# Optimization experiments

Hardware: AMD Instinct MI355X
Metric: run time of the kernel (lower is better)

## Reference

```python
import jax, jax.numpy as jnp
import numpy as np

CUTOFF = 4.0
RBF_N = 32          # distance_embedding_size == D_rbf
F_DIM = 128         # hidden_size
N_ATOMS = 20000
N_PROBES = 100000
N_EDGES = 262144
LN_EPS = 1e-5


def setup_inputs() -> dict:
    key = jax.random.key(0)
    ks = jax.random.split(key, 20)
    s = 0.02
    inp = {
        "diff_pi": jax.random.normal(ks[0], (N_EDGES, 3), jnp.float32),
        "S_JK": jax.random.normal(ks[1], (N_ATOMS, F_DIM), jnp.float32),
        "V_JK": jax.random.normal(ks[2], (N_ATOMS, 3, F_DIM), jnp.float32),
        "atom_idx": jax.random.randint(ks[3], (N_EDGES,), 0, N_ATOMS),
        "probe_idx": jax.random.randint(ks[4], (N_EDGES,), 0, N_PROBES),
        "num_probes": N_PROBES,
        # state branch params
        "w_s1": jax.random.normal(ks[5], (3 * F_DIM, F_DIM), jnp.float32) * s,
        "b_s1": jnp.zeros((F_DIM,), jnp.float32),
        "g_ln": jnp.ones((F_DIM,), jnp.float32),
        "b_ln": jnp.zeros((F_DIM,), jnp.float32),
        "w_s2": jax.random.normal(ks[6], (F_DIM, F_DIM), jnp.float32) * s,
        "b_s2": jnp.zeros((F_DIM,), jnp.float32),
        # filter branch params
        "w_f1": jax.random.normal(ks[7], (RBF_N, F_DIM), jnp.float32) * s,
        "b_f1": jnp.zeros((F_DIM,), jnp.float32),
        "w_f2": jax.random.normal(ks[8], (F_DIM, F_DIM), jnp.float32) * s,
        "b_f2": jnp.zeros((F_DIM,), jnp.float32),
        # output head params
        "w_o1": jax.random.normal(ks[9], (F_DIM, F_DIM // 2), jnp.float32) * s,
        "b_o1": jnp.zeros((F_DIM // 2,), jnp.float32),
        "w_o2": jax.random.normal(ks[10], (F_DIM // 2, 1), jnp.float32) * s,
        "b_o2": jnp.zeros((1,), jnp.float32),
        "final_bias": jnp.array([-6.1], jnp.float32),
    }
    return inp


def reference(diff_pi, S_JK, V_JK, atom_idx, probe_idx, num_probes,
              w_s1, b_s1, g_ln, b_ln, w_s2, b_s2,
              w_f1, b_f1, w_f2, b_f2,
              w_o1, b_o1, w_o2, b_o2, final_bias):
    silu = jax.nn.silu
    # edge distances
    sq = (diff_pi ** 2).sum(-1)                       # [E]
    dist = jnp.sqrt(sq)                               # [E] exact distance
    dist_safe = jnp.sqrt(sq + 1e-8)[:, None]          # [E,1]
    r_hat = diff_pi / dist_safe                       # [E,3]

    # sinc RBF expansion: sin(n*pi*d/cutoff)/d, n=1..RBF_N
    n = jnp.arange(1, RBF_N + 1, dtype=diff_pi.dtype) # [D]
    e_pi = jnp.sin(dist[:, None] * n * (jnp.pi / CUTOFF)) / dist[:, None]  # [E,D]

    # gather atom features to edges
    n_i = jnp.sqrt((V_JK ** 2).sum(1) + 1e-8)         # [N,F]
    n_e = n_i[atom_idx]                               # [E,F]
    V_e = V_JK[atom_idx]                              # [E,3,F]
    q_pi = (V_e * r_hat[:, :, None]).sum(1)           # [E,F]
    S_e = S_JK[atom_idx]                              # [E,F]

    # state branch: Linear -> LayerNorm -> SiLU -> Linear
    h = jnp.concatenate([S_e, n_e, q_pi], axis=-1)    # [E,3F]
    u = h @ w_s1 + b_s1                               # [E,F]
    mu = u.mean(-1, keepdims=True)
    var = ((u - mu) ** 2).mean(-1, keepdims=True)
    u_norm = (u - mu) / jnp.sqrt(var + LN_EPS) * g_ln + b_ln
    state = silu(u_norm) @ w_s2 + b_s2                # [E,F]

    # filter branch (no normalization -> absolute distance scale)
    W = silu(e_pi @ w_f1 + b_f1) @ w_f2 + b_f2        # [E,F]

    # fuse + output head
    m = (silu((W * state) @ w_o1 + b_o1) @ w_o2 + b_o2)[:, 0]  # [E]

    x = dist / CUTOFF
    env = 1.0 - 21.0 * x ** 5 + 35.0 * x ** 6 - 15.0 * x ** 7
    env = jnp.where(dist < CUTOFF, env, jnp.zeros_like(env))
    m_w = m * env

    # scatter-add to probes
    rho = jax.ops.segment_sum(m_w, probe_idx, num_segments=num_probes)
    return rho + final_bias[0]
```

## Files before the change

kernel.cpp:

```cpp
#include <hip/hip_runtime.h>

#define EPB     64
#define E_TOTAL 262144
#define NPROBE  100000
#define N_ATOMS 20000
#define NTAB    4096

#define ASTR   136
#define A2_O   0
#define S_O    8704
#define MPT_O  17408
#define LDS_SH 17920

#define WS1_O  0
#define WS2_O  49152
#define WO1_O  65536
#define WT_TOT 73728
#define PQ_O   73728
#define PQ_SH  (N_ATOMS * 512)
#define WTAB_OFF_B ((PQ_O + PQ_SH) * 2)

typedef __attribute__((ext_vector_type(8))) short          short8;
typedef __attribute__((ext_vector_type(8))) unsigned short ushort8;
typedef __attribute__((ext_vector_type(4))) float          floatx4;

#define MFMA16(a, b, c) __builtin_amdgcn_mfma_f32_16x16x32_bf16((a), (b), (c), 0, 0, 0)

__device__ __forceinline__ short f2bf(float x) {
    unsigned u = __builtin_bit_cast(unsigned, x);
    u = (u + 0x7FFFu + ((u >> 16) & 1u)) >> 16;
    return (short)(unsigned short)u;
}
__device__ __forceinline__ unsigned pk2(float lo, float hi) {
    return __builtin_amdgcn_perm(__builtin_bit_cast(unsigned, hi),
                                 __builtin_bit_cast(unsigned, lo), 0x07060302u);
}
__device__ __forceinline__ float bf2f(unsigned short u) {
    return __builtin_bit_cast(float, ((unsigned)u) << 16);
}
__device__ __forceinline__ float silu_f(float x) { return x / (1.0f + __expf(-x)); }

struct F8 { float v[8]; };
__device__ __forceinline__ F8 ld8(const float* __restrict__ p) {
    F8 r;
    const float4 a = *(const float4*)p;
    const float4 b = *(const float4*)(p + 4);
    r.v[0] = a.x; r.v[1] = a.y; r.v[2] = a.z; r.v[3] = a.w;
    r.v[4] = b.x; r.v[5] = b.y; r.v[6] = b.z; r.v[7] = b.w;
    return r;
}

__global__ void cfr_prep_w(const float* __restrict__ w_s1, const float* __restrict__ w_s2,
                           const float* __restrict__ w_o1,
                           const float* __restrict__ fb, float* __restrict__ out,
                           unsigned short* __restrict__ wt) {
    int i = blockIdx.x * 256 + threadIdx.x;
    if (i < NPROBE) out[i] = fb[0];
    if (i < WT_TOT) {
        float v;
        if (i < WS2_O)      { int n = i / 384, k = i - n * 384;          v = w_s1[k * 128 + n]; }
        else if (i < WO1_O) { int j = i - WS2_O, n = j >> 7, k = j & 127; v = w_s2[k * 128 + n]; }
        else                { int j = i - WO1_O, n = j >> 7, k = j & 127; v = w_o1[k * 64 + n]; }
        wt[i] = (unsigned short)f2bf(v);
    }
}

__global__ __launch_bounds__(128) void cfr_prep_wtab(
    const float* __restrict__ w_f1, const float* __restrict__ b_f1,
    const float* __restrict__ w_f2, const float* __restrict__ b_f2,
    float* __restrict__ wtab)
{
    __shared__ float ep[32];
    __shared__ float f1s[128];
    const int t = threadIdx.x, row = blockIdx.x;
    float d = fmaxf(row * (4.0f / NTAB), 1e-4f);
    if (t < 32) ep[t] = sinf(d * (t + 1) * 0.7853981633974483f) / d;
    __syncthreads();
    float f1 = b_f1[t];
#pragma unroll
    for (int k = 0; k < 32; ++k) f1 = fmaf(ep[k], w_f1[k * 128 + t], f1);
    f1s[t] = silu_f(f1);
    __syncthreads();
    float w = b_f2[t];
    for (int k = 0; k < 128; ++k) w = fmaf(f1s[k], w_f2[k * 128 + t], w);
    wtab[row * 128 + t] = w;
}

__global__ __launch_bounds__(256, 3) void cfr_prep_pq(
    const float* __restrict__ S, const float* __restrict__ V,
    const float* __restrict__ b_s1,
    const unsigned short* __restrict__ wt, unsigned short* __restrict__ pq)
{
    __shared__ __align__(16) unsigned short bufH[32 * 264];
    __shared__ __align__(16) unsigned short bufV[96 * 136];

    const int t    = threadIdx.x;
    const int a0   = blockIdx.x * 32;
    const int wave = t >> 6;
    const int lane = t & 63;
    const int q    = lane >> 4;
    const int c16  = lane & 15;

#pragma unroll
    for (int it = 0; it < 2; ++it) {
        int idx = it * 256 + t;
        int al = idx >> 4, f8 = (idx & 15) * 8;
        int a = a0 + al;
        ushort8 sS, sN, s0, s1, s2;
        if (a < N_ATOMS) {
            F8 s  = ld8(S + a * 128 + f8);
            F8 v0 = ld8(V + a * 384 + f8);
            F8 v1 = ld8(V + a * 384 + 128 + f8);
            F8 v2 = ld8(V + a * 384 + 256 + f8);
#pragma unroll
            for (int j = 0; j < 8; ++j) {
                sS[j] = (unsigned short)f2bf(s.v[j]);
                sN[j] = (unsigned short)f2bf(sqrtf(v0.v[j]*v0.v[j] + v1.v[j]*v1.v[j] + v2.v[j]*v2.v[j] + 1e-8f));
                s0[j] = (unsigned short)f2bf(v0.v[j]);
                s1[j] = (unsigned short)f2bf(v1.v[j]);
                s2[j] = (unsigned short)f2bf(v2.v[j]);
            }
        } else {
#pragma unroll
            for (int j = 0; j < 8; ++j) { sS[j]=0; sN[j]=0; s0[j]=0; s1[j]=0; s2[j]=0; }
        }
        *(ushort8*)&bufH[al * 264 + f8]        = sS;
        *(ushort8*)&bufH[al * 264 + 128 + f8]  = sN;
        *(ushort8*)&bufV[al * 136 + f8]        = s0;
        *(ushort8*)&bufV[(32 + al) * 136 + f8] = s1;
        *(ushort8*)&bufV[(64 + al) * 136 + f8] = s2;
    }
    __syncthreads();

    const floatx4 zero4 = {0.f, 0.f, 0.f, 0.f};
    float bs1c[2];
#pragma unroll
    for (int ni = 0; ni < 2; ++ni) bs1c[ni] = b_s1[wave * 32 + ni * 16 + c16];

    {
        floatx4 pacc[2][2];
#pragma unroll
        for (int mi = 0; mi < 2; ++mi) { pacc[mi][0] = zero4; pacc[mi][1] = zero4; }
#pragma unroll
        for (int kk = 0; kk < 8; ++kk) {
            short8 bfr[2], af[2];
#pragma unroll
            for (int ni = 0; ni < 2; ++ni) {
                int n = wave * 32 + ni * 16 + c16;
                bfr[ni] = *(const short8*)&wt[WS1_O + n * 384 + kk * 32 + q * 8];
            }
#pragma unroll
            for (int mi = 0; mi < 2; ++mi)
                af[mi] = *(const short8*)&bufH[(mi * 16 + c16) * 264 + kk * 32 + q * 8];
#pragma unroll
            for (int mi = 0; mi < 2; ++mi)
#pragma unroll
                for (int ni = 0; ni < 2; ++ni)
                    pacc[mi][ni] = MFMA16(af[mi], bfr[ni], pacc[mi][ni]);
        }
#pragma unroll
        for (int mi = 0; mi < 2; ++mi)
#pragma unroll
            for (int r = 0; r < 4; ++r) {
                int a = a0 + mi * 16 + q * 4 + r;
                if (a < N_ATOMS)
#pragma unroll
                    for (int ni = 0; ni < 2; ++ni) {
                        int col = wave * 32 + ni * 16 + c16;
                        pq[a * 512 + col] = (unsigned short)f2bf(pacc[mi][ni][r] + bs1c[ni]);
                    }
            }
    }

    short8 bq[4][2];
#pragma unroll
    for (int kk = 0; kk < 4; ++kk)
#pragma unroll
        for (int ni = 0; ni < 2; ++ni) {
            int n = wave * 32 + ni * 16 + c16;
            bq[kk][ni] = *(const short8*)&wt[WS1_O + n * 384 + 256 + kk * 32 + q * 8];
        }
#pragma unroll
    for (int d = 0; d < 3; ++d) {
        floatx4 qacc[2][2];
#pragma unroll
        for (int mi = 0; mi < 2; ++mi) { qacc[mi][0] = zero4; qacc[mi][1] = zero4; }
#pragma unroll
        for (int kk = 0; kk < 4; ++kk) {
            short8 af[2];
#pragma unroll
            for (int mi = 0; mi < 2; ++mi)
                af[mi] = *(const short8*)&bufV[(d * 32 + mi * 16 + c16) * 136 + kk * 32 + q * 8];
#pragma unroll
            for (int mi = 0; mi < 2; ++mi)
#pragma unroll
                for (int ni = 0; ni < 2; ++ni)
                    qacc[mi][ni] = MFMA16(af[mi], bq[kk][ni], qacc[mi][ni]);
        }
#pragma unroll
        for (int mi = 0; mi < 2; ++mi)
#pragma unroll
            for (int r = 0; r < 4; ++r) {
                int a = a0 + mi * 16 + q * 4 + r;
                if (a < N_ATOMS)
#pragma unroll
                    for (int ni = 0; ni < 2; ++ni) {
                        int col = wave * 32 + ni * 16 + c16;
                        pq[a * 512 + (1 + d) * 128 + col] = (unsigned short)f2bf(qacc[mi][ni][r]);
                    }
            }
    }
}

__global__ __launch_bounds__(256, 4) void cfr_main(
    const float* __restrict__ diff,
    const int* __restrict__ atom_idx, const int* __restrict__ probe_idx,
    const unsigned short* __restrict__ wt, const unsigned short* __restrict__ pq,
    const float* __restrict__ wtab,
    const float* __restrict__ g_ln, const float* __restrict__ b_ln,
    const float* __restrict__ b_s2, const float* __restrict__ b_o1,
    const float* __restrict__ w_o2, const float* __restrict__ b_o2,
    float* __restrict__ out)
{
    __shared__ __align__(16) unsigned short LDSu[LDS_SH];
    float* mpart = (float*)&LDSu[MPT_O];

    const int t    = threadIdx.x;
    const int e0   = blockIdx.x * EPB;
    const int wave = t >> 6;
    const int lane = t & 63;
    const int q    = lane >> 4;
    const int c16  = lane & 15;
    const floatx4 zero4 = {0.f, 0.f, 0.f, 0.f};

    const int el = t >> 2;
    const int c0 = (t & 3) * 32;
    float dist;

    {
        const int eg = e0 + el;
        const int a  = atom_idx[eg];
        float dx = diff[eg * 3 + 0], dy = diff[eg * 3 + 1], dz = diff[eg * 3 + 2];
        float sq = dx * dx + dy * dy + dz * dz;
        dist = sqrtf(sq);
        float rinv = rsqrtf(sq + 1e-8f);
        float rx = dx * rinv, ry = dy * rinv, rz = dz * rinv;

        const ushort8* pqr = (const ushort8*)(pq + a * 512 + c0);
        float u[32];
#pragma unroll
        for (int g = 0; g < 4; ++g) {
            ushort8 v = pqr[g];
#pragma unroll
            for (int j = 0; j < 8; ++j) u[g * 8 + j] = bf2f(v[j]);
        }
#pragma unroll
        for (int g = 0; g < 4; ++g) {
            ushort8 v = pqr[16 + g];
#pragma unroll
            for (int j = 0; j < 8; ++j) u[g * 8 + j] = fmaf(bf2f(v[j]), rx, u[g * 8 + j]);
        }
#pragma unroll
        for (int g = 0; g < 4; ++g) {
            ushort8 v = pqr[32 + g];
#pragma unroll
            for (int j = 0; j < 8; ++j) u[g * 8 + j] = fmaf(bf2f(v[j]), ry, u[g * 8 + j]);
        }
#pragma unroll
        for (int g = 0; g < 4; ++g) {
            ushort8 v = pqr[48 + g];
#pragma unroll
            for (int j = 0; j < 8; ++j) u[g * 8 + j] = fmaf(bf2f(v[j]), rz, u[g * 8 + j]);
        }
        float s = 0.f, s2 = 0.f;
#pragma unroll
        for (int j = 0; j < 32; ++j) { s += u[j]; s2 = fmaf(u[j], u[j], s2); }
        s  += __shfl_xor(s, 1);  s  += __shfl_xor(s, 2);
        s2 += __shfl_xor(s2, 1); s2 += __shfl_xor(s2, 2);
        float mu = s * (1.f / 128.f);
        float rstd = rsqrtf(s2 * (1.f / 128.f) - mu * mu + 1e-5f);
        const float4* gp = (const float4*)(g_ln + c0);
        const float4* bp = (const float4*)(b_ln + c0);
        unsigned pko[16];
#pragma unroll
        for (int g4 = 0; g4 < 8; ++g4) {
            float4 gg = gp[g4], bb = bp[g4];
            float y0 = silu_f((u[g4 * 4 + 0] - mu) * rstd * gg.x + bb.x);
            float y1 = silu_f((u[g4 * 4 + 1] - mu) * rstd * gg.y + bb.y);
            float y2 = silu_f((u[g4 * 4 + 2] - mu) * rstd * gg.z + bb.z);
            float y3 = silu_f((u[g4 * 4 + 3] - mu) * rstd * gg.w + bb.w);
            pko[g4 * 2 + 0] = pk2(y0, y1);
            pko[g4 * 2 + 1] = pk2(y2, y3);
        }
        uint4* dst = (uint4*)&LDSu[A2_O + el * ASTR + c0];
        dst[0] = make_uint4(pko[0], pko[1], pko[2], pko[3]);
        dst[1] = make_uint4(pko[4], pko[5], pko[6], pko[7]);
        dst[2] = make_uint4(pko[8], pko[9], pko[10], pko[11]);
        dst[3] = make_uint4(pko[12], pko[13], pko[14], pko[15]);
    }
    __syncthreads();

    {
        floatx4 sacc[4][2];
#pragma unroll
        for (int mi = 0; mi < 4; ++mi) { sacc[mi][0] = zero4; sacc[mi][1] = zero4; }
#pragma unroll
        for (int kk = 0; kk < 4; ++kk) {
            short8 a2f[4], b2[2];
#pragma unroll
            for (int ni = 0; ni < 2; ++ni) {
                int n = wave * 32 + ni * 16 + c16;
                b2[ni] = *(const short8*)&wt[WS2_O + n * 128 + kk * 32 + q * 8];
            }
#pragma unroll
            for (int mi = 0; mi < 4; ++mi)
                a2f[mi] = *(const short8*)&LDSu[A2_O + (mi * 16 + c16) * ASTR + kk * 32 + q * 8];
#pragma unroll
            for (int mi = 0; mi < 4; ++mi)
#pragma unroll
                for (int ni = 0; ni < 2; ++ni)
                    sacc[mi][ni] = MFMA16(a2f[mi], b2[ni], sacc[mi][ni]);
        }
        float bs2c[2];
#pragma unroll
        for (int ni = 0; ni < 2; ++ni) bs2c[ni] = b_s2[wave * 32 + ni * 16 + c16];
#pragma unroll
        for (int mi = 0; mi < 4; ++mi)
#pragma unroll
            for (int r = 0; r < 4; ++r) {
                int row = mi * 16 + q * 4 + r;
#pragma unroll
                for (int ni = 0; ni < 2; ++ni) {
                    float v = sacc[mi][ni][r] + bs2c[ni];
                    LDSu[S_O + row * ASTR + (wave * 32 + ni * 16 + c16)] =
                        (unsigned short)(__builtin_bit_cast(unsigned, v) >> 16);
                }
            }
    }
    __syncthreads();

    {
        float f  = fminf(dist * (NTAB / 4.0f), (float)(NTAB - 1));
        float fi = floorf(f);
        int   i0 = (int)fi;
        float fr = f - fi;
        const float* r0 = wtab + i0 * 128 + c0;
        const float* r1 = r0 + 128;
        float w0[32], w1[32];
#pragma unroll
        for (int g4 = 0; g4 < 8; ++g4) {
            *(float4*)&w0[g4 * 4] = *(const float4*)(r0 + g4 * 4);
            *(float4*)&w1[g4 * 4] = *(const float4*)(r1 + g4 * 4);
        }
        ushort8 sv[4];
#pragma unroll
        for (int g = 0; g < 4; ++g)
            sv[g] = *(const ushort8*)&LDSu[S_O + el * ASTR + c0 + g * 8];
        unsigned pko[16];
#pragma unroll
        for (int p = 0; p < 16; ++p) {
            int j0 = p * 2, j1 = p * 2 + 1;
            float wa = fmaf(fr, w1[j0] - w0[j0], w0[j0]);
            float wb = fmaf(fr, w1[j1] - w0[j1], w0[j1]);
            float ga = bf2f(sv[j0 >> 3][j0 & 7]) * wa;
            float gb = bf2f(sv[j1 >> 3][j1 & 7]) * wb;
            pko[p] = pk2(ga, gb);
        }
        uint4* dst = (uint4*)&LDSu[A2_O + el * ASTR + c0];
        dst[0] = make_uint4(pko[0], pko[1], pko[2], pko[3]);
        dst[1] = make_uint4(pko[4], pko[5], pko[6], pko[7]);
        dst[2] = make_uint4(pko[8], pko[9], pko[10], pko[11]);
        dst[3] = make_uint4(pko[12], pko[13], pko[14], pko[15]);
    }
    __syncthreads();

    {
        const int n2 = wave * 16 + c16;
        floatx4 oacc[4];
#pragma unroll
        for (int mi = 0; mi < 4; ++mi) oacc[mi] = zero4;
#pragma unroll
        for (int kk = 0; kk < 4; ++kk) {
            short8 bfr = *(const short8*)&wt[WO1_O + n2 * 128 + kk * 32 + q * 8];
#pragma unroll
            for (int mi = 0; mi < 4; ++mi) {
                short8 af = *(const short8*)&LDSu[A2_O + (mi * 16 + c16) * ASTR + kk * 32 + q * 8];
                oacc[mi] = MFMA16(af, bfr, oacc[mi]);
            }
        }
        float bo1c = b_o1[n2], wo2c = w_o2[n2];
#pragma unroll
        for (int mi = 0; mi < 4; ++mi)
#pragma unroll
            for (int r = 0; r < 4; ++r) {
                float s = silu_f(oacc[mi][r] + bo1c) * wo2c;
#pragma unroll
                for (int d = 1; d < 16; d <<= 1) s += __shfl_xor(s, d, 64);
                if (c16 == 0) mpart[(mi * 16 + q * 4 + r) * 4 + wave] = s;
            }
    }
    __syncthreads();

    if (t < EPB) {
        int eg = e0 + t;
        float m = mpart[t * 4 + 0] + mpart[t * 4 + 1] + mpart[t * 4 + 2] + mpart[t * 4 + 3] + b_o2[0];
        float dx = diff[eg * 3 + 0], dy = diff[eg * 3 + 1], dz = diff[eg * 3 + 2];
        float dd = sqrtf(dx * dx + dy * dy + dz * dz);
        float x  = dd * 0.25f;
        float x2 = x * x, x4 = x2 * x2;
        float x5 = x4 * x, x6 = x5 * x, x7 = x6 * x;
        float env = 1.0f - 21.0f * x5 + 35.0f * x6 - 15.0f * x7;
        env = (dd < 4.0f) ? env : 0.0f;
        float mw = m * env;
        if (mw != 0.f) unsafeAtomicAdd(&out[probe_idx[eg]], mw);
    }
}

extern "C" void kernel_launch(void* const* d_in, const int* in_sizes, int n_in,
                              void* d_out, int out_size, void* d_ws, size_t ws_size,
                              hipStream_t stream) {
    const float* diff    = (const float*)d_in[0];
    const float* S_JK    = (const float*)d_in[1];
    const float* V_JK    = (const float*)d_in[2];
    const int*   atom_i  = (const int*)d_in[3];
    const int*   probe_i = (const int*)d_in[4];
    const float* w_s1 = (const float*)d_in[6];
    const float* b_s1 = (const float*)d_in[7];
    const float* g_ln = (const float*)d_in[8];
    const float* b_ln = (const float*)d_in[9];
    const float* w_s2 = (const float*)d_in[10];
    const float* b_s2 = (const float*)d_in[11];
    const float* w_f1 = (const float*)d_in[12];
    const float* b_f1 = (const float*)d_in[13];
    const float* w_f2 = (const float*)d_in[14];
    const float* b_f2 = (const float*)d_in[15];
    const float* w_o1 = (const float*)d_in[16];
    const float* b_o1 = (const float*)d_in[17];
    const float* w_o2 = (const float*)d_in[18];
    const float* b_o2 = (const float*)d_in[19];
    const float* fbias = (const float*)d_in[20];
    float* out = (float*)d_out;

    unsigned short* wt  = (unsigned short*)d_ws;
    unsigned short* pqp = wt + PQ_O;
    float* wtab = (float*)((char*)d_ws + WTAB_OFF_B);

    cfr_prep_w<<<(NPROBE + 255) / 256, 256, 0, stream>>>(w_s1, w_s2, w_o1, fbias, out, wt);
    cfr_prep_wtab<<<NTAB + 1, 128, 0, stream>>>(w_f1, b_f1, w_f2, b_f2, wtab);
    cfr_prep_pq<<<(N_ATOMS + 31) / 32, 256, 0, stream>>>(S_JK, V_JK, b_s1, wt, pqp);
    cfr_main<<<E_TOTAL / EPB, 256, 0, stream>>>(diff, atom_i, probe_i, wt, pqp, wtab,
        g_ln, b_ln, b_s2, b_o1, w_o2, b_o2, out);
}
```

Baseline: 249.8 us.

## Sort edges by atom, pack bf16 filter table pairs, fuse filter into epilogue

Adds a counting sort of the edges by atom index (histogram, scan, scatter) so the per-edge gathers of the precomputed atom projections are grouped in memory. Diff and probe index are packed together into a float4 per sorted edge. The filter table is halved in size and stored as packed bf16 pairs of adjacent rows. The filter interpolation and multiply now happen directly in the state GEMM epilogue, which removes an LDS staging buffer and allows higher occupancy. The cost is four extra small kernels, extra workspace, lower table precision and a less spread-out pattern of atomics.

```diff
diff --git a/kernel.cpp b/kernel.cpp
--- a/kernel.cpp
+++ b/kernel.cpp
@@ -4,21 +4,23 @@
 #define E_TOTAL 262144
 #define NPROBE  100000
 #define N_ATOMS 20000
-#define NTAB    4096
+#define NTAB    2048
 
 #define ASTR   136
 #define A2_O   0
-#define S_O    8704
-#define MPT_O  17408
-#define LDS_SH 17920
+#define LDS_SH 8704
 
 #define WS1_O  0
 #define WS2_O  49152
 #define WO1_O  65536
 #define WT_TOT 73728
-#define PQ_O   73728
-#define PQ_SH  (N_ATOMS * 512)
-#define WTAB_OFF_B ((PQ_O + PQ_SH) * 2)
+#define PQ_B   147456
+#define WTI_B  20627456
+#define WTF_B  21676032
+#define CNT_B  22725120
+#define CUR_B  22805120
+#define SA_B   22885120
+#define ED_B   23933696
 
 typedef __attribute__((ext_vector_type(8))) short          short8;
 typedef __attribute__((ext_vector_type(8))) unsigned short ushort8;
@@ -26,10 +28,10 @@
 
 #define MFMA16(a, b, c) __builtin_amdgcn_mfma_f32_16x16x32_bf16((a), (b), (c), 0, 0, 0)
 
-__device__ __forceinline__ short f2bf(float x) {
+__device__ __forceinline__ unsigned short f2bfu(float x) {
     unsigned u = __builtin_bit_cast(unsigned, x);
     u = (u + 0x7FFFu + ((u >> 16) & 1u)) >> 16;
-    return (short)(unsigned short)u;
+    return (unsigned short)u;
 }
 __device__ __forceinline__ unsigned pk2(float lo, float hi) {
     return __builtin_amdgcn_perm(__builtin_bit_cast(unsigned, hi),
@@ -53,22 +55,67 @@
 __global__ void cfr_prep_w(const float* __restrict__ w_s1, const float* __restrict__ w_s2,
                            const float* __restrict__ w_o1,
                            const float* __restrict__ fb, float* __restrict__ out,
-                           unsigned short* __restrict__ wt) {
+                           unsigned short* __restrict__ wt, int* __restrict__ cnt) {
     int i = blockIdx.x * 256 + threadIdx.x;
     if (i < NPROBE) out[i] = fb[0];
+    if (i < N_ATOMS) cnt[i] = 0;
     if (i < WT_TOT) {
         float v;
         if (i < WS2_O)      { int n = i / 384, k = i - n * 384;          v = w_s1[k * 128 + n]; }
         else if (i < WO1_O) { int j = i - WS2_O, n = j >> 7, k = j & 127; v = w_s2[k * 128 + n]; }
         else                { int j = i - WO1_O, n = j >> 7, k = j & 127; v = w_o1[k * 64 + n]; }
-        wt[i] = (unsigned short)f2bf(v);
-    }
+        wt[i] = f2bfu(v);
+    }
+}
+
+__global__ void cfr_hist(const int* __restrict__ atom_idx, int* __restrict__ cnt) {
+    int e = blockIdx.x * 256 + threadIdx.x;
+    if (e < E_TOTAL) atomicAdd(&cnt[atom_idx[e]], 1);
+}
+
+__global__ __launch_bounds__(1024) void cfr_scan(const int* __restrict__ cnt,
+                                                 int* __restrict__ cur) {
+    __shared__ int part[1024];
+    const int t = threadIdx.x, base = t * 20;
+    int loc[20]; int s = 0;
+#pragma unroll
+    for (int i = 0; i < 20; ++i) {
+        int v = (base + i < N_ATOMS) ? cnt[base + i] : 0;
+        loc[i] = s; s += v;
+    }
+    part[t] = s;
+    __syncthreads();
+    for (int d = 1; d < 1024; d <<= 1) {
+        int v = (t >= d) ? part[t - d] : 0;
+        __syncthreads();
+        part[t] += v;
+        __syncthreads();
+    }
+    int pre = (t == 0) ? 0 : part[t - 1];
+#pragma unroll
+    for (int i = 0; i < 20; ++i)
+        if (base + i < N_ATOMS) cur[base + i] = pre + loc[i];
+}
+
+__global__ void cfr_scatter(const int* __restrict__ atom_idx, const int* __restrict__ probe_idx,
+                            const float* __restrict__ diff,
+                            int* __restrict__ cur, int* __restrict__ sortedA,
+                            float4* __restrict__ ediff) {
+    int e = blockIdx.x * 256 + threadIdx.x;
+    if (e >= E_TOTAL) return;
+    int a = atom_idx[e];
+    int pos = atomicAdd(&cur[a], 1);
+    sortedA[pos] = a;
+    float4 ed;
+    ed.x = diff[e * 3 + 0]; ed.y = diff[e * 3 + 1]; ed.z = diff[e * 3 + 2];
+    ed.w = __int_as_float(probe_idx[e]);
+    ediff[pos] = ed;
 }
 
 __global__ __launch_bounds__(128) void cfr_prep_wtab(
     const float* __restrict__ w_f1, const float* __restrict__ b_f1,
     const float* __restrict__ w_f2, const float* __restrict__ b_f2,
-    float* __restrict__ wtab)
+    float* __restrict__ wtabF)
 {
     __shared__ float ep[32];
     __shared__ float f1s[128];
@@ -82,8 +129,19 @@
     f1s[t] = silu_f(f1);
     __syncthreads();
     float w = b_f2[t];
+#pragma unroll 4
     for (int k = 0; k < 128; ++k) w = fmaf(f1s[k], w_f2[k * 128 + t], w);
-    wtab[row * 128 + t] = w;
+    wtabF[row * 128 + t] = w;
+}
+
+__global__ void cfr_prep_wtab_pack(const float* __restrict__ wtabF,
+                                   unsigned* __restrict__ wtabI) {
+    int i = blockIdx.x * 256 + threadIdx.x;
+    if (i >= NTAB * 128) return;
+    int r = i >> 7, c = i & 127;
+    unsigned lo = f2bfu(wtabF[r * 128 + c]);
+    unsigned hi = f2bfu(wtabF[(r + 1) * 128 + c]);
+    wtabI[i] = (hi << 16) | lo;
 }
 
 __global__ __launch_bounds__(256, 3) void cfr_prep_pq(
@@ -114,11 +172,11 @@
             F8 v2 = ld8(V + a * 384 + 256 + f8);
 #pragma unroll
             for (int j = 0; j < 8; ++j) {
-                sS[j] = (unsigned short)f2bf(s.v[j]);
-                sN[j] = (unsigned short)f2bf(sqrtf(v0.v[j]*v0.v[j] + v1.v[j]*v1.v[j] + v2.v[j]*v2.v[j] + 1e-8f));
-                s0[j] = (unsigned short)f2bf(v0.v[j]);
-                s1[j] = (unsigned short)f2bf(v1.v[j]);
-                s2[j] = (unsigned short)f2bf(v2.v[j]);
+                sS[j] = f2bfu(s.v[j]);
+                sN[j] = f2bfu(sqrtf(v0.v[j]*v0.v[j] + v1.v[j]*v1.v[j] + v2.v[j]*v2.v[j] + 1e-8f));
+                s0[j] = f2bfu(v0.v[j]);
+                s1[j] = f2bfu(v1.v[j]);
+                s2[j] = f2bfu(v2.v[j]);
             }
         } else {
 #pragma unroll
@@ -167,7 +225,7 @@
 #pragma unroll
                     for (int ni = 0; ni < 2; ++ni) {
                         int col = wave * 32 + ni * 16 + c16;
-                        pq[a * 512 + col] = (unsigned short)f2bf(pacc[mi][ni][r] + bs1c[ni]);
+                        pq[a * 512 + col] = f2bfu(pacc[mi][ni][r] + bs1c[ni]);
                     }
             }
     }
@@ -206,24 +264,25 @@
 #pragma unroll
                     for (int ni = 0; ni < 2; ++ni) {
                         int col = wave * 32 + ni * 16 + c16;
-                        pq[a * 512 + (1 + d) * 128 + col] = (unsigned short)f2bf(qacc[mi][ni][r]);
+                        pq[a * 512 + (1 + d) * 128 + col] = f2bfu(qacc[mi][ni][r]);
                     }
             }
     }
 }
 
-__global__ __launch_bounds__(256, 4) void cfr_main(
-    const float* __restrict__ diff,
-    const int* __restrict__ atom_idx, const int* __restrict__ probe_idx,
+__global__ __launch_bounds__(256, 8) void cfr_main(
+    const int* __restrict__ aidx, const float4* __restrict__ ediff,
     const unsigned short* __restrict__ wt, const unsigned short* __restrict__ pq,
-    const float* __restrict__ wtab,
+    const unsigned* __restrict__ wtabI,
     const float* __restrict__ g_ln, const float* __restrict__ b_ln,
     const float* __restrict__ b_s2, const float* __restrict__ b_o1,
     const float* __restrict__ w_o2, const float* __restrict__ b_o2,
     float* __restrict__ out)
 {
     __shared__ __align__(16) unsigned short LDSu[LDS_SH];
-    float* mpart = (float*)&LDSu[MPT_O];
+    __shared__ float df[EPB];
+    __shared__ int   probe_s[EPB];
+    __shared__ float mpart[EPB * 4];
 
     const int t    = threadIdx.x;
     const int e0   = blockIdx.x * EPB;
@@ -235,16 +294,16 @@
 
     const int el = t >> 2;
     const int c0 = (t & 3) * 32;
-    float dist;
 
     {
         const int eg = e0 + el;
-        const int a  = atom_idx[eg];
-        float dx = diff[eg * 3 + 0], dy = diff[eg * 3 + 1], dz = diff[eg * 3 + 2];
-        float sq = dx * dx + dy * dy + dz * dz;
-        dist = sqrtf(sq);
+        const int a  = aidx[eg];
+        float4 ed = ediff[eg];
+        float sq = ed.x * ed.x + ed.y * ed.y + ed.z * ed.z;
+        float dist = sqrtf(sq);
         float rinv = rsqrtf(sq + 1e-8f);
-        float rx = dx * rinv, ry = dy * rinv, rz = dz * rinv;
+        float rx = ed.x * rinv, ry = ed.y * rinv, rz = ed.z * rinv;
+        if ((t & 3) == 0) { df[el] = dist; probe_s[el] = __float_as_int(ed.w); }
 
         const ushort8* pqr = (const ushort8*)(pq + a * 512 + c0);
         float u[32];
@@ -321,56 +380,34 @@
                 for (int ni = 0; ni < 2; ++ni)
                     sacc[mi][ni] = MFMA16(a2f[mi], b2[ni], sacc[mi][ni]);
         }
+        __syncthreads();
+
         float bs2c[2];
 #pragma unroll
         for (int ni = 0; ni < 2; ++ni) bs2c[ni] = b_s2[wave * 32 + ni * 16 + c16];
 #pragma unroll
-        for (int mi = 0; mi < 4; ++mi)
+        for (int mi = 0; mi < 4; ++mi) {
 #pragma unroll
             for (int r = 0; r < 4; ++r) {
                 int row = mi * 16 + q * 4 + r;
+                float f  = fminf(df[row] * (NTAB / 4.0f), NTAB - 1.01f);
+                float fi = floorf(f);
+                int   i0 = (int)fi;
+                float fr = f - fi;
+                const unsigned* wrow = wtabI + i0 * 128;
 #pragma unroll
                 for (int ni = 0; ni < 2; ++ni) {
-                    float v = sacc[mi][ni][r] + bs2c[ni];
-                    LDSu[S_O + row * ASTR + (wave * 32 + ni * 16 + c16)] =
-                        (unsigned short)(__builtin_bit_cast(unsigned, v) >> 16);
+                    int col = wave * 32 + ni * 16 + c16;
+                    unsigned wp = wrow[col];
+                    float w0 = __builtin_bit_cast(float, wp << 16);
+                    float w1 = __builtin_bit_cast(float, wp & 0xffff0000u);
+                    float wv = fmaf(fr, w1 - w0, w0);
+                    float g  = (sacc[mi][ni][r] + bs2c[ni]) * wv;
+                    LDSu[A2_O + row * ASTR + col] =
+                        (unsigned short)(__builtin_bit_cast(unsigned, g) >> 16);
                 }
             }
-    }
-    __syncthreads();
-
-    {
-        float f  = fminf(dist * (NTAB / 4.0f), (float)(NTAB - 1));
-        float fi = floorf(f);
-        int   i0 = (int)fi;
-        float fr = f - fi;
-        const float* r0 = wtab + i0 * 128 + c0;
-        const float* r1 = r0 + 128;
-        float w0[32], w1[32];
-#pragma unroll
-        for (int g4 = 0; g4 < 8; ++g4) {
-            *(float4*)&w0[g4 * 4] = *(const float4*)(r0 + g4 * 4);
-            *(float4*)&w1[g4 * 4] = *(const float4*)(r1 + g4 * 4);
-        }
-        ushort8 sv[4];
-#pragma unroll
-        for (int g = 0; g < 4; ++g)
-            sv[g] = *(const ushort8*)&LDSu[S_O + el * ASTR + c0 + g * 8];
-        unsigned pko[16];
-#pragma unroll
-        for (int p = 0; p < 16; ++p) {
-            int j0 = p * 2, j1 = p * 2 + 1;
-            float wa = fmaf(fr, w1[j0] - w0[j0], w0[j0]);
-            float wb = fmaf(fr, w1[j1] - w0[j1], w0[j1]);
-            float ga = bf2f(sv[j0 >> 3][j0 & 7]) * wa;
-            float gb = bf2f(sv[j1 >> 3][j1 & 7]) * wb;
-            pko[p] = pk2(ga, gb);
-        }
-        uint4* dst = (uint4*)&LDSu[A2_O + el * ASTR + c0];
-        dst[0] = make_uint4(pko[0], pko[1], pko[2], pko[3]);
-        dst[1] = make_uint4(pko[4], pko[5], pko[6], pko[7]);
-        dst[2] = make_uint4(pko[8], pko[9], pko[10], pko[11]);
-        dst[3] = make_uint4(pko[12], pko[13], pko[14], pko[15]);
+        }
     }
     __syncthreads();
 
@@ -402,17 +439,15 @@
     __syncthreads();
 
     if (t < EPB) {
-        int eg = e0 + t;
         float m = mpart[t * 4 + 0] + mpart[t * 4 + 1] + mpart[t * 4 + 2] + mpart[t * 4 + 3] + b_o2[0];
-        float dx = diff[eg * 3 + 0], dy = diff[eg * 3 + 1], dz = diff[eg * 3 + 2];
-        float dd = sqrtf(dx * dx + dy * dy + dz * dz);
+        float dd = df[t];
         float x  = dd * 0.25f;
         float x2 = x * x, x4 = x2 * x2;
         float x5 = x4 * x, x6 = x5 * x, x7 = x6 * x;
         float env = 1.0f - 21.0f * x5 + 35.0f * x6 - 15.0f * x7;
         env = (dd < 4.0f) ? env : 0.0f;
         float mw = m * env;
-        if (mw != 0.f) unsafeAtomicAdd(&out[probe_idx[eg]], mw);
+        if (mw != 0.f) unsafeAtomicAdd(&out[probe_s[t]], mw);
     }
 }
 
@@ -441,13 +476,23 @@
     const float* fbias = (const float*)d_in[20];
     float* out = (float*)d_out;
 
-    unsigned short* wt  = (unsigned short*)d_ws;
-    unsigned short* pqp = wt + PQ_O;
-    float* wtab = (float*)((char*)d_ws + WTAB_OFF_B);
-
-    cfr_prep_w<<<(NPROBE + 255) / 256, 256, 0, stream>>>(w_s1, w_s2, w_o1, fbias, out, wt);
-    cfr_prep_wtab<<<NTAB + 1, 128, 0, stream>>>(w_f1, b_f1, w_f2, b_f2, wtab);
+    char* ws = (char*)d_ws;
+    unsigned short* wt    = (unsigned short*)ws;
+    unsigned short* pqp   = (unsigned short*)(ws + PQ_B);
+    unsigned*       wtabI = (unsigned*)(ws + WTI_B);
+    float*          wtabF = (float*)(ws + WTF_B);
+    int*            cnt   = (int*)(ws + CNT_B);
+    int*            cur   = (int*)(ws + CUR_B);
+    int*            srtA  = (int*)(ws + SA_B);
+    float4*         edif  = (float4*)(ws + ED_B);
+
+    cfr_prep_w<<<(NPROBE + 255) / 256, 256, 0, stream>>>(w_s1, w_s2, w_o1, fbias, out, wt, cnt);
+    cfr_hist<<<E_TOTAL / 256, 256, 0, stream>>>(atom_i, cnt);
+    cfr_scan<<<1, 1024, 0, stream>>>(cnt, cur);
+    cfr_scatter<<<E_TOTAL / 256, 256, 0, stream>>>(atom_i, probe_i, diff, cur, srtA, edif);
+    cfr_prep_wtab<<<NTAB + 1, 128, 0, stream>>>(w_f1, b_f1, w_f2, b_f2, wtabF);
+    cfr_prep_wtab_pack<<<(NTAB * 128) / 256, 256, 0, stream>>>(wtabF, wtabI);
     cfr_prep_pq<<<(N_ATOMS + 31) / 32, 256, 0, stream>>>(S_JK, V_JK, b_s1, wt, pqp);
-    cfr_main<<<E_TOTAL / EPB, 256, 0, stream>>>(diff, atom_i, probe_i, wt, pqp, wtab,
+    cfr_main<<<E_TOTAL / EPB, 256, 0, stream>>>(srtA, edif, wt, pqp, wtabI,
         g_ln, b_ln, b_s2, b_o1, w_o2, b_o2, out);
 }
```

Measured after the change: 290.1 us. 16.1% more time.
